# Kernel optimization log

Hardware: AMD Instinct MI355X
Metric: run time of the kernel (lower is better)

The kernel has to match this reference:

```python
import jax, jax.numpy as jnp
import numpy as np

COST_CLASS = 2.0
COST_MASK = 5.0
COST_DICE = 5.0
NUM_POINTS = 12544


def _point_sample(masks, coords):
    """Bilinear sample masks [N,H,W] at coords [P,2] in [0,1] (x,y order),
    matching F.grid_sample(align_corners=False, padding_mode='zeros')."""
    H, W = masks.shape[-2], masks.shape[-1]
    x = coords[:, 0] * W - 0.5  # [P]
    y = coords[:, 1] * H - 0.5
    x0 = jnp.floor(x)
    y0 = jnp.floor(y)
    wx = (x - x0).astype(masks.dtype)
    wy = (y - y0).astype(masks.dtype)
    x0i = x0.astype(jnp.int32)
    y0i = y0.astype(jnp.int32)

    def gather(xi, yi):
        valid = ((xi >= 0) & (xi < W) & (yi >= 0) & (yi < H)).astype(masks.dtype)
        xc = jnp.clip(xi, 0, W - 1)
        yc = jnp.clip(yi, 0, H - 1)
        return masks[:, yc, xc] * valid[None, :]  # [N,P]

    v00 = gather(x0i, y0i)
    v01 = gather(x0i + 1, y0i)
    v10 = gather(x0i, y0i + 1)
    v11 = gather(x0i + 1, y0i + 1)
    return (v00 * (1 - wx) * (1 - wy) + v01 * wx * (1 - wy)
            + v10 * (1 - wx) * wy + v11 * wx * wy)  # [N,P]


def setup_inputs() -> dict:
    key = jax.random.key(0)
    ks = jax.random.split(key, 6)
    B, Q, C, T, H, W = 8, 100, 41, 50, 256, 256
    return {
        "pred_logits": jax.random.normal(ks[0], (B, Q, C), jnp.float32),
        "pred_object_logits": jax.random.normal(ks[1], (B, Q, 2), jnp.float32),
        "pred_masks": jax.random.normal(ks[2], (B, Q, H, W), jnp.float32),
        "tgt_masks": jax.random.uniform(ks[3], (B, T, H, W), jnp.float32),
        "tgt_labels": jax.random.randint(ks[4], (B, T), 0, C),
        "point_coords": jax.random.uniform(ks[5], (B, NUM_POINTS, 2), jnp.float32),
    }


def reference(pred_logits, pred_object_logits, pred_masks, tgt_masks, tgt_labels, point_coords):
    B, Q, C = pred_logits.shape
    T = tgt_labels.shape[1]
    P = point_coords.shape[1]

    # --- class cost ---
    out_class_prob = jax.nn.sigmoid(pred_logits[..., :-1])          # [B,Q,C-1]
    out_object_prob = jax.nn.softmax(pred_object_logits, axis=-1)   # [B,Q,2]
    out_prob = jnp.concatenate(
        [jnp.sqrt(out_class_prob * out_object_prob[..., 0:1]),
         out_object_prob[..., 1:2]], axis=-1)                       # [B,Q,C]
    idx = jnp.broadcast_to(tgt_labels[:, None, :], (B, Q, T))
    cost_class = -jnp.take_along_axis(out_prob, idx, axis=2)        # [B,Q,T]

    # --- point-sample masks at shared random points ---
    om = jax.vmap(_point_sample)(pred_masks, point_coords)          # [B,Q,P]
    tm = jax.vmap(_point_sample)(tgt_masks, point_coords)           # [B,T,P]

    # --- batched sigmoid CE cost ---
    pos = jax.nn.softplus(-om)  # BCE vs target=1
    neg = jax.nn.softplus(om)   # BCE vs target=0
    cost_mask = (jnp.einsum('bqp,btp->bqt', pos, tm)
                 + jnp.einsum('bqp,btp->bqt', neg, 1.0 - tm)) / P

    # --- batched dice cost ---
    s = jax.nn.sigmoid(om)
    numerator = 2.0 * jnp.einsum('bqp,btp->bqt', s, tm)
    denominator = s.sum(-1)[:, :, None] + tm.sum(-1)[:, None, :]
    cost_dice = 1.0 - (numerator + 1.0) / (denominator + 1.0)

    Cmat = COST_MASK * cost_mask + COST_CLASS * cost_class + COST_DICE * cost_dice
    return Cmat  # [B,Q,T] batched assignment cost matrices
```

## Files before the change

### kernel.cpp

```cpp
#include <hip/hip_runtime.h>
#include <math.h>

#define BB 8
#define QQ 100
#define CC 41
#define TT 50
#define HH 256
#define WW 256
#define PP 12544
#define QP 112
#define TP 64
#define KS 8
#define KCH (PP / KS)

typedef _Float16 f16x8 __attribute__((ext_vector_type(8)));
typedef float f32x4 __attribute__((ext_vector_type(4)));

#if defined(__has_builtin)
#if __has_builtin(__builtin_amdgcn_cvt_pk_fp8_f32) && __has_builtin(__builtin_amdgcn_cvt_f32_fp8)
#define HAVE_FP8CVT 1
#endif
#endif

__device__ __forceinline__ unsigned int cvt1_e4m3_sw(float x) {
    unsigned int u = __float_as_uint(x);
    unsigned int s = (u >> 24) & 0x80u;
    float ax = fminf(fabsf(x), 448.f);
    if (ax < 0.015625f) {
        unsigned int m = (unsigned int)rintf(ax * 512.f);
        return s | m;
    }
    unsigned int v = __float_as_uint(ax);
    v += 0x7FFFFu + ((v >> 20) & 1u);
    int e = (int)(v >> 23) - 127;
    unsigned int m = (v >> 20) & 7u;
    if (e < -6) { m = (unsigned int)rintf(ax * 512.f); return s | m; }
    unsigned int ee = (unsigned int)(e + 7);
    if (ee >= 16u) { ee = 15u; m = 6u; }
    return s | (ee << 3) | m;
}

template <bool HI>
__device__ __forceinline__ unsigned int pack2_e4m3(float a, float b, unsigned int old) {
#ifdef HAVE_FP8CVT
    return (unsigned int)__builtin_amdgcn_cvt_pk_fp8_f32(a, b, (int)old, HI);
#else
    unsigned int p = (cvt1_e4m3_sw(a) | (cvt1_e4m3_sw(b) << 8)) << (HI ? 16 : 0);
    unsigned int mask = HI ? 0x0000FFFFu : 0xFFFF0000u;
    return (old & mask) | p;
#endif
}

__device__ __forceinline__ float e4m3_to_f32(unsigned int byte) {
#ifdef HAVE_FP8CVT
    return __builtin_amdgcn_cvt_f32_fp8((int)byte, 0);
#else
    unsigned int s = byte >> 7, e = (byte >> 3) & 15u, m = byte & 7u;
    float v = e ? __uint_as_float(((e + 120u) << 23) | (m << 20))
                : (float)m * 0.001953125f;
    return s ? -v : v;
#endif
}

__device__ __forceinline__ float samp(const unsigned char* __restrict__ mlds, float2 c) {
    float x = fmaf(c.x, 256.f, -0.5f);
    float y = fmaf(c.y, 256.f, -0.5f);
    float x0f = floorf(x), y0f = floorf(y);
    float wx = x - x0f, wy = y - y0f;
    int x0 = (int)x0f, y0 = (int)y0f;
    float fx0 = (x0 >= 0) ? 1.f : 0.f, fx1 = (x0 < 255) ? 1.f : 0.f;
    float fy0 = (y0 >= 0) ? 1.f : 0.f, fy1 = (y0 < 255) ? 1.f : 0.f;
    int x0c = max(x0, 0), x1c = min(x0 + 1, 255);
    int r0 = max(y0, 0) << 8, r1 = (min(y0 + 1, 255)) << 8;
    float v00 = e4m3_to_f32(mlds[r0 + x0c]);
    float v01 = e4m3_to_f32(mlds[r0 + x1c]);
    float v10 = e4m3_to_f32(mlds[r1 + x0c]);
    float v11 = e4m3_to_f32(mlds[r1 + x1c]);
    float wxa = (1.f - wx) * fx0, wxb = wx * fx1;
    float wya = (1.f - wy) * fy0, wyb = wy * fy1;
    return wya * fmaf(wxa, v00, wxb * v01) + wyb * fmaf(wxa, v10, wxb * v11);
}

__global__ __launch_bounds__(1024, 8) void sample_kernel(
    const float* __restrict__ tgt_masks, const float* __restrict__ pred_masks,
    const float* __restrict__ coords,
    _Float16* __restrict__ tm, _Float16* __restrict__ om, _Float16* __restrict__ sg,
    float* __restrict__ tmsum, float* __restrict__ nsum, float* __restrict__ ssum)
{
    __shared__ unsigned char mlds[HH * WW];
    __shared__ float red[16], red2[16];
    int id = blockIdx.x;
    int tid = threadIdx.x;
    bool is_t = id < BB * TT;
    int b;
    const float* m;
    _Float16* dst;
    _Float16* dsg = nullptr;
    if (is_t) {
        b = id / TT;
        m = tgt_masks + (size_t)id * (HH * WW);
        dst = tm + ((size_t)b * TP + (id % TT)) * PP;
    } else {
        int bq = id - BB * TT;
        b = bq / QQ;
        int q = bq % QQ;
        m = pred_masks + (size_t)bq * (HH * WW);
        dst = om + ((size_t)b * QP + q) * PP;
        dsg = sg + ((size_t)b * QP + q) * PP;
    }
    const float2* cd = (const float2*)coords + (size_t)b * PP;

    {
        const float4* s4 = (const float4*)m;
        unsigned int* dl = (unsigned int*)mlds;
        float4 v0 = s4[tid], v1 = s4[tid + 1024], v2 = s4[tid + 2048], v3 = s4[tid + 3072];
        float4 v4 = s4[tid + 4096], v5 = s4[tid + 5120], v6 = s4[tid + 6144], v7 = s4[tid + 7168];
        unsigned int pk;
        pk = pack2_e4m3<false>(v0.x, v0.y, 0u); dl[tid]        = pack2_e4m3<true>(v0.z, v0.w, pk);
        pk = pack2_e4m3<false>(v1.x, v1.y, 0u); dl[tid + 1024] = pack2_e4m3<true>(v1.z, v1.w, pk);
        pk = pack2_e4m3<false>(v2.x, v2.y, 0u); dl[tid + 2048] = pack2_e4m3<true>(v2.z, v2.w, pk);
        pk = pack2_e4m3<false>(v3.x, v3.y, 0u); dl[tid + 3072] = pack2_e4m3<true>(v3.z, v3.w, pk);
        pk = pack2_e4m3<false>(v4.x, v4.y, 0u); dl[tid + 4096] = pack2_e4m3<true>(v4.z, v4.w, pk);
        pk = pack2_e4m3<false>(v5.x, v5.y, 0u); dl[tid + 5120] = pack2_e4m3<true>(v5.z, v5.w, pk);
        pk = pack2_e4m3<false>(v6.x, v6.y, 0u); dl[tid + 6144] = pack2_e4m3<true>(v6.z, v6.w, pk);
        pk = pack2_e4m3<false>(v7.x, v7.y, 0u); dl[tid + 7168] = pack2_e4m3<true>(v7.z, v7.w, pk);
        float4 u0 = s4[tid + 8192], u1 = s4[tid + 9216], u2 = s4[tid + 10240], u3 = s4[tid + 11264];
        float4 u4 = s4[tid + 12288], u5 = s4[tid + 13312], u6 = s4[tid + 14336], u7 = s4[tid + 15360];
        pk = pack2_e4m3<false>(u0.x, u0.y, 0u); dl[tid + 8192]  = pack2_e4m3<true>(u0.z, u0.w, pk);
        pk = pack2_e4m3<false>(u1.x, u1.y, 0u); dl[tid + 9216]  = pack2_e4m3<true>(u1.z, u1.w, pk);
        pk = pack2_e4m3<false>(u2.x, u2.y, 0u); dl[tid + 10240] = pack2_e4m3<true>(u2.z, u2.w, pk);
        pk = pack2_e4m3<false>(u3.x, u3.y, 0u); dl[tid + 11264] = pack2_e4m3<true>(u3.z, u3.w, pk);
        pk = pack2_e4m3<false>(u4.x, u4.y, 0u); dl[tid + 12288] = pack2_e4m3<true>(u4.z, u4.w, pk);
        pk = pack2_e4m3<false>(u5.x, u5.y, 0u); dl[tid + 13312] = pack2_e4m3<true>(u5.z, u5.w, pk);
        pk = pack2_e4m3<false>(u6.x, u6.y, 0u); dl[tid + 14336] = pack2_e4m3<true>(u6.z, u6.w, pk);
        pk = pack2_e4m3<false>(u7.x, u7.y, 0u); dl[tid + 15360] = pack2_e4m3<true>(u7.z, u7.w, pk);
    }
    __syncthreads();

    float sA = 0.f, sB = 0.f;
    float nA = 0.f, nB = 0.f;
    float gA = 0.f, gB = 0.f;

    if (is_t) {
        #pragma unroll
        for (int g = 0; g < 3; ++g) {
            int p0 = g * 4096 + tid;
            float2 c0 = cd[p0], c1 = cd[p0 + 1024], c2 = cd[p0 + 2048], c3 = cd[p0 + 3072];
            float v0 = samp(mlds, c0), v1 = samp(mlds, c1);
            float v2 = samp(mlds, c2), v3 = samp(mlds, c3);
            dst[p0] = (_Float16)v0;
            dst[p0 + 1024] = (_Float16)v1;
            dst[p0 + 2048] = (_Float16)v2;
            dst[p0 + 3072] = (_Float16)v3;
            sA += v0 + v2; sB += v1 + v3;
        }
        if (tid < 256) {
            int p = 12288 + tid;
            float v = samp(mlds, cd[p]);
            dst[p] = (_Float16)v;
            sA += v;
        }
    } else {
        #pragma unroll
        for (int g = 0; g < 3; ++g) {
            int p0 = g * 4096 + tid;
            float2 c0 = cd[p0], c1 = cd[p0 + 1024], c2 = cd[p0 + 2048], c3 = cd[p0 + 3072];
            float v0 = samp(mlds, c0), v1 = samp(mlds, c1);
            float v2 = samp(mlds, c2), v3 = samp(mlds, c3);
            dst[p0] = (_Float16)v0;
            dst[p0 + 1024] = (_Float16)v1;
            dst[p0 + 2048] = (_Float16)v2;
            dst[p0 + 3072] = (_Float16)v3;
            float e0 = __expf(-fabsf(v0)), e1 = __expf(-fabsf(v1));
            float e2 = __expf(-fabsf(v2)), e3 = __expf(-fabsf(v3));
            float r0 = 1.f / (1.f + e0), r1 = 1.f / (1.f + e1);
            float r2 = 1.f / (1.f + e2), r3 = 1.f / (1.f + e3);
            float g0 = (v0 >= 0.f) ? r0 : e0 * r0, g1 = (v1 >= 0.f) ? r1 : e1 * r1;
            float g2 = (v2 >= 0.f) ? r2 : e2 * r2, g3 = (v3 >= 0.f) ? r3 : e3 * r3;
            dsg[p0] = (_Float16)g0;
            dsg[p0 + 1024] = (_Float16)g1;
            dsg[p0 + 2048] = (_Float16)g2;
            dsg[p0 + 3072] = (_Float16)g3;
            nA += fmaxf(v0, 0.f) + __logf(1.f + e0) + fmaxf(v2, 0.f) + __logf(1.f + e2);
            nB += fmaxf(v1, 0.f) + __logf(1.f + e1) + fmaxf(v3, 0.f) + __logf(1.f + e3);
            gA += g0 + g2; gB += g1 + g3;
        }
        if (tid < 256) {
            int p = 12288 + tid;
            float v = samp(mlds, cd[p]);
            dst[p] = (_Float16)v;
            float e = __expf(-fabsf(v));
            float r = 1.f / (1.f + e);
            float gg = (v >= 0.f) ? r : e * r;
            dsg[p] = (_Float16)gg;
            nA += fmaxf(v, 0.f) + __logf(1.f + e);
            gA += gg;
        }
    }

    float l1 = is_t ? (sA + sB) : (nA + nB);
    float l2 = gA + gB;
    #pragma unroll
    for (int off = 32; off; off >>= 1) {
        l1 += __shfl_down(l1, off, 64);
        l2 += __shfl_down(l2, off, 64);
    }
    if ((tid & 63) == 0) { red[tid >> 6] = l1; red2[tid >> 6] = l2; }
    __syncthreads();
    if (tid == 0) {
        float t1 = 0.f, t2 = 0.f;
        #pragma unroll
        for (int w = 0; w < 16; ++w) { t1 += red[w]; t2 += red2[w]; }
        if (is_t) tmsum[id] = t1;
        else { nsum[id - BB * TT] = t1; ssum[id - BB * TT] = t2; }
    }
}

__global__ __launch_bounds__(256) void dot_mfma_kernel(
    const _Float16* __restrict__ om, const _Float16* __restrict__ sg,
    const _Float16* __restrict__ tm,
    float* __restrict__ part_om, float* __restrict__ part_s)
{
    int qt = blockIdx.x, b = blockIdx.y, ks = blockIdx.z;
    int tid = threadIdx.x, lane = tid & 63, w = tid >> 6;
    int ra = lane & 15;
    int ko = (lane >> 4) * 8;
    const _Float16* pa = om + ((size_t)(b * QP + qt * 16 + ra)) * PP + ks * KCH + ko;
    const _Float16* ps = sg + ((size_t)(b * QP + qt * 16 + ra)) * PP + ks * KCH + ko;
    const _Float16* pb = tm + ((size_t)(b * TP + w * 16 + ra)) * PP + ks * KCH + ko;
    f32x4 accO = {0.f, 0.f, 0.f, 0.f};
    f32x4 accS = {0.f, 0.f, 0.f, 0.f};
    #pragma unroll 7
    for (int k = 0; k < KCH / 32; ++k) {
        f16x8 a = *(const f16x8*)(pa + (size_t)k * 32);
        f16x8 s = *(const f16x8*)(ps + (size_t)k * 32);
        f16x8 bb = *(const f16x8*)(pb + (size_t)k * 32);
        accO = __builtin_amdgcn_mfma_f32_16x16x32_f16(a, bb, accO, 0, 0, 0);
        accS = __builtin_amdgcn_mfma_f32_16x16x32_f16(s, bb, accS, 0, 0, 0);
    }
    int t = w * 16 + ra;
    int q = qt * 16 + (lane >> 4) * 4;
    size_t base = (((size_t)ks * BB + b) * QP + q) * TP + t;
    #pragma unroll
    for (int r = 0; r < 4; ++r) {
        part_om[base + (size_t)r * TP] = accO[r];
        part_s[base + (size_t)r * TP] = accS[r];
    }
}

__global__ __launch_bounds__(256) void epilogue_kernel(
    const float* __restrict__ part_om, const float* __restrict__ part_s,
    const float* __restrict__ tmsum, const float* __restrict__ nsum,
    const float* __restrict__ ssum, const float* __restrict__ pred_logits,
    const float* __restrict__ pred_obj, const int* __restrict__ labels,
    float* __restrict__ out)
{
    int i = blockIdx.x * 256 + threadIdx.x;
    if (i >= BB * QQ * TT) return;
    int t = i % TT;
    int bq = i / TT;
    int b = bq / QQ, q = bq % QQ;
    float dO = 0.f, dS = 0.f;
    #pragma unroll
    for (int ks = 0; ks < KS; ++ks) {
        size_t o = (((size_t)ks * BB + b) * QP + q) * TP + t;
        dO += part_om[o];
        dS += part_s[o];
    }
    float ns = nsum[bq], ss = ssum[bq];
    float ts = tmsum[b * TT + t];
    float cmask = (ns - dO) * (1.f / PP);
    float cdice = 1.f - (2.f * dS + 1.f) / (ss + ts + 1.f);
    int label = labels[b * TT + t];
    float a0 = pred_obj[bq * 2], a1 = pred_obj[bq * 2 + 1];
    float prob;
    if (label == CC - 1) {
        prob = 1.f / (1.f + __expf(a0 - a1));
    } else {
        float pc = 1.f / (1.f + __expf(-pred_logits[(size_t)bq * CC + label]));
        float po = 1.f / (1.f + __expf(a1 - a0));
        prob = sqrtf(pc * po);
    }
    out[i] = 5.f * cmask - 2.f * prob + 5.f * cdice;
}

extern "C" void kernel_launch(void* const* d_in, const int* in_sizes, int n_in,
                              void* d_out, int out_size, void* d_ws, size_t ws_size,
                              hipStream_t stream) {
    const float* pred_logits = (const float*)d_in[0];
    const float* pred_obj    = (const float*)d_in[1];
    const float* pred_masks  = (const float*)d_in[2];
    const float* tgt_masks   = (const float*)d_in[3];
    const int*   tgt_labels  = (const int*)d_in[4];
    const float* coords      = (const float*)d_in[5];
    float* out = (float*)d_out;

    char* ws = (char*)d_ws;
    const size_t SZ_OM = (size_t)BB * QP * PP * 2;
    const size_t SZ_TM = (size_t)BB * TP * PP * 2;
    const size_t SZ_PT = (size_t)KS * BB * QP * TP * 4;
    _Float16* om  = (_Float16*)ws;
    _Float16* sg  = (_Float16*)(ws + SZ_OM);
    _Float16* tmm = (_Float16*)(ws + 2 * SZ_OM);
    float* part_om = (float*)(ws + 2 * SZ_OM + SZ_TM);
    float* part_s  = (float*)(ws + 2 * SZ_OM + SZ_TM + SZ_PT);
    float* tmsum   = (float*)(ws + 2 * SZ_OM + SZ_TM + 2 * SZ_PT);
    float* nsum    = tmsum + BB * TT;
    float* ssum    = nsum + BB * QQ;

    hipLaunchKernelGGL(sample_kernel, dim3(BB * TT + BB * QQ), dim3(1024), 0, stream,
                       tgt_masks, pred_masks, coords, tmm, om, sg, tmsum, nsum, ssum);
    hipLaunchKernelGGL(dot_mfma_kernel, dim3(QP / 16, BB, KS), dim3(256), 0, stream,
                       om, sg, tmm, part_om, part_s);
    hipLaunchKernelGGL(epilogue_kernel, dim3((BB * QQ * TT + 255) / 256), dim3(256),
                       0, stream,
                       part_om, part_s, tmsum, nsum, ssum,
                       pred_logits, pred_obj, tgt_labels, out);
}
```

Before: 120.3 us.

## Make sample kernel persistent with double-buffered LDS prefetch of next mask

Each block of the sampling kernel now processes five masks in sequence using two 64KB LDS buffers. It loads the next mask from global memory into registers while sampling the current one, then packs it to fp8 into the other buffer. The aim is to overlap the global mask reads with gather/sampling compute. In exchange, LDS per block doubles, limiting residency to one block per CU, and the grid shrinks to 240 blocks, which may leave CUs idle.

Measured after the change: 124.4 us. 3.5% more time.

```diff
diff --git a/kernel.cpp b/kernel.cpp
--- a/kernel.cpp
+++ b/kernel.cpp
@@ -5,13 +5,15 @@
 #define QQ 100
 #define CC 41
 #define TT 50
-#define HH 256
-#define WW 256
 #define PP 12544
 #define QP 112
 #define TP 64
 #define KS 8
 #define KCH (PP / KS)
+#define NT (BB * TT)
+#define NMASK (NT + BB * QQ)
+#define MPB 5
+#define SGRID (NMASK / MPB)
 
 typedef _Float16 f16x8 __attribute__((ext_vector_type(8)));
 typedef float f32x4 __attribute__((ext_vector_type(4)));
@@ -62,7 +64,8 @@
 #endif
 }
 
-__device__ __forceinline__ float samp(const unsigned char* __restrict__ mlds, float2 c) {
+__device__ __forceinline__ void addr_w(float2 c, int& a00, int& a01, int& a10, int& a11,
+                                       float& xa, float& xb, float& ya, float& yb) {
     float x = fmaf(c.x, 256.f, -0.5f);
     float y = fmaf(c.y, 256.f, -0.5f);
     float x0f = floorf(x), y0f = floorf(y);
@@ -71,148 +74,152 @@
     float fx0 = (x0 >= 0) ? 1.f : 0.f, fx1 = (x0 < 255) ? 1.f : 0.f;
     float fy0 = (y0 >= 0) ? 1.f : 0.f, fy1 = (y0 < 255) ? 1.f : 0.f;
     int x0c = max(x0, 0), x1c = min(x0 + 1, 255);
-    int r0 = max(y0, 0) << 8, r1 = (min(y0 + 1, 255)) << 8;
-    float v00 = e4m3_to_f32(mlds[r0 + x0c]);
-    float v01 = e4m3_to_f32(mlds[r0 + x1c]);
-    float v10 = e4m3_to_f32(mlds[r1 + x0c]);
-    float v11 = e4m3_to_f32(mlds[r1 + x1c]);
-    float wxa = (1.f - wx) * fx0, wxb = wx * fx1;
-    float wya = (1.f - wy) * fy0, wyb = wy * fy1;
-    return wya * fmaf(wxa, v00, wxb * v01) + wyb * fmaf(wxa, v10, wxb * v11);
-}
-
-__global__ __launch_bounds__(1024, 8) void sample_kernel(
+    int r0 = max(y0, 0) << 8, r1 = min(y0 + 1, 255) << 8;
+    a00 = r0 + x0c; a01 = r0 + x1c; a10 = r1 + x0c; a11 = r1 + x1c;
+    xa = (1.f - wx) * fx0; xb = wx * fx1;
+    ya = (1.f - wy) * fy0; yb = wy * fy1;
+}
+
+__global__ __launch_bounds__(1024, 4) void sample_kernel(
     const float* __restrict__ tgt_masks, const float* __restrict__ pred_masks,
     const float* __restrict__ coords,
     _Float16* __restrict__ tm, _Float16* __restrict__ om, _Float16* __restrict__ sg,
     float* __restrict__ tmsum, float* __restrict__ nsum, float* __restrict__ ssum)
 {
-    __shared__ unsigned char mlds[HH * WW];
+    __shared__ unsigned int buf[2][16384];
     __shared__ float red[16], red2[16];
-    int id = blockIdx.x;
     int tid = threadIdx.x;
-    bool is_t = id < BB * TT;
-    int b;
-    const float* m;
-    _Float16* dst;
-    _Float16* dsg = nullptr;
-    if (is_t) {
-        b = id / TT;
-        m = tgt_masks + (size_t)id * (HH * WW);
-        dst = tm + ((size_t)b * TP + (id % TT)) * PP;
-    } else {
-        int bq = id - BB * TT;
-        b = bq / QQ;
-        int q = bq % QQ;
-        m = pred_masks + (size_t)bq * (HH * WW);
-        dst = om + ((size_t)b * QP + q) * PP;
-        dsg = sg + ((size_t)b * QP + q) * PP;
-    }
-    const float2* cd = (const float2*)coords + (size_t)b * PP;
+    int base = blockIdx.x * MPB;
 
     {
-        const float4* s4 = (const float4*)m;
-        unsigned int* dl = (unsigned int*)mlds;
-        float4 v0 = s4[tid], v1 = s4[tid + 1024], v2 = s4[tid + 2048], v3 = s4[tid + 3072];
-        float4 v4 = s4[tid + 4096], v5 = s4[tid + 5120], v6 = s4[tid + 6144], v7 = s4[tid + 7168];
-        unsigned int pk;
-        pk = pack2_e4m3<false>(v0.x, v0.y, 0u); dl[tid]        = pack2_e4m3<true>(v0.z, v0.w, pk);
-        pk = pack2_e4m3<false>(v1.x, v1.y, 0u); dl[tid + 1024] = pack2_e4m3<true>(v1.z, v1.w, pk);
-        pk = pack2_e4m3<false>(v2.x, v2.y, 0u); dl[tid + 2048] = pack2_e4m3<true>(v2.z, v2.w, pk);
-        pk = pack2_e4m3<false>(v3.x, v3.y, 0u); dl[tid + 3072] = pack2_e4m3<true>(v3.z, v3.w, pk);
-        pk = pack2_e4m3<false>(v4.x, v4.y, 0u); dl[tid + 4096] = pack2_e4m3<true>(v4.z, v4.w, pk);
-        pk = pack2_e4m3<false>(v5.x, v5.y, 0u); dl[tid + 5120] = pack2_e4m3<true>(v5.z, v5.w, pk);
-        pk = pack2_e4m3<false>(v6.x, v6.y, 0u); dl[tid + 6144] = pack2_e4m3<true>(v6.z, v6.w, pk);
-        pk = pack2_e4m3<false>(v7.x, v7.y, 0u); dl[tid + 7168] = pack2_e4m3<true>(v7.z, v7.w, pk);
-        float4 u0 = s4[tid + 8192], u1 = s4[tid + 9216], u2 = s4[tid + 10240], u3 = s4[tid + 11264];
-        float4 u4 = s4[tid + 12288], u5 = s4[tid + 13312], u6 = s4[tid + 14336], u7 = s4[tid + 15360];
-        pk = pack2_e4m3<false>(u0.x, u0.y, 0u); dl[tid + 8192]  = pack2_e4m3<true>(u0.z, u0.w, pk);
-        pk = pack2_e4m3<false>(u1.x, u1.y, 0u); dl[tid + 9216]  = pack2_e4m3<true>(u1.z, u1.w, pk);
-        pk = pack2_e4m3<false>(u2.x, u2.y, 0u); dl[tid + 10240] = pack2_e4m3<true>(u2.z, u2.w, pk);
-        pk = pack2_e4m3<false>(u3.x, u3.y, 0u); dl[tid + 11264] = pack2_e4m3<true>(u3.z, u3.w, pk);
-        pk = pack2_e4m3<false>(u4.x, u4.y, 0u); dl[tid + 12288] = pack2_e4m3<true>(u4.z, u4.w, pk);
-        pk = pack2_e4m3<false>(u5.x, u5.y, 0u); dl[tid + 13312] = pack2_e4m3<true>(u5.z, u5.w, pk);
-        pk = pack2_e4m3<false>(u6.x, u6.y, 0u); dl[tid + 14336] = pack2_e4m3<true>(u6.z, u6.w, pk);
-        pk = pack2_e4m3<false>(u7.x, u7.y, 0u); dl[tid + 15360] = pack2_e4m3<true>(u7.z, u7.w, pk);
+        const float* m0 = (base < NT) ? tgt_masks + (size_t)base * 65536
+                                      : pred_masks + (size_t)(base - NT) * 65536;
+        const float4* s4 = (const float4*)m0;
+        for (int half = 0; half < 2; ++half) {
+            float4 r[8];
+            #pragma unroll
+            for (int k = 0; k < 8; ++k) r[k] = s4[half * 8192 + k * 1024 + tid];
+            #pragma unroll
+            for (int k = 0; k < 8; ++k) {
+                unsigned int pk = pack2_e4m3<false>(r[k].x, r[k].y, 0u);
+                buf[0][half * 8192 + k * 1024 + tid] = pack2_e4m3<true>(r[k].z, r[k].w, pk);
+            }
+        }
     }
     __syncthreads();
 
-    float sA = 0.f, sB = 0.f;
-    float nA = 0.f, nB = 0.f;
-    float gA = 0.f, gB = 0.f;
-
-    if (is_t) {
+    for (int j = 0; j < MPB; ++j) {
+        int id = base + j;
+        bool is_t = id < NT;
+        int b;
+        _Float16* dst;
+        _Float16* dsg = nullptr;
+        if (is_t) {
+            b = id / TT;
+            dst = tm + ((size_t)b * TP + (id % TT)) * PP;
+        } else {
+            int bq = id - NT;
+            b = bq / QQ;
+            dst = om + ((size_t)b * QP + (bq % QQ)) * PP;
+            dsg = sg + ((size_t)b * QP + (bq % QQ)) * PP;
+        }
+        const float2* cd = (const float2*)coords + (size_t)b * PP;
+        const unsigned char* curb = (const unsigned char*)buf[j & 1];
+        unsigned int* nxt = buf[(j + 1) & 1];
+        bool has_next = (j + 1 < MPB);
+        const float4* ns4 = nullptr;
+        if (has_next) {
+            int nid = id + 1;
+            ns4 = (const float4*)((nid < NT) ? tgt_masks + (size_t)nid * 65536
+                                             : pred_masks + (size_t)(nid - NT) * 65536);
+        }
+
+        float l1 = 0.f, l2 = 0.f;
+        for (int half = 0; half < 2; ++half) {
+            float4 r[8];
+            if (has_next) {
+                #pragma unroll
+                for (int k = 0; k < 8; ++k) r[k] = ns4[half * 8192 + k * 1024 + tid];
+            }
+            #pragma unroll
+            for (int pr = 0; pr < 3; ++pr) {
+                int p1 = (half * 6 + pr * 2) * 1024 + tid;
+                int p2 = p1 + 1024;
+                float2 c1 = cd[p1], c2 = cd[p2];
+                int a00, a01, a10, a11, e00, e01, e10, e11;
+                float xa1, xb1, ya1, yb1, xa2, xb2, ya2, yb2;
+                addr_w(c1, a00, a01, a10, a11, xa1, xb1, ya1, yb1);
+                addr_w(c2, e00, e01, e10, e11, xa2, xb2, ya2, yb2);
+                unsigned int u00 = curb[a00], u01 = curb[a01];
+                unsigned int u10 = curb[a10], u11 = curb[a11];
+                unsigned int w00 = curb[e00], w01 = curb[e01];
+                unsigned int w10 = curb[e10], w11 = curb[e11];
+                float v1 = ya1 * fmaf(xa1, e4m3_to_f32(u00), xb1 * e4m3_to_f32(u01))
+                         + yb1 * fmaf(xa1, e4m3_to_f32(u10), xb1 * e4m3_to_f32(u11));
+                float v2 = ya2 * fmaf(xa2, e4m3_to_f32(w00), xb2 * e4m3_to_f32(w01))
+                         + yb2 * fmaf(xa2, e4m3_to_f32(w10), xb2 * e4m3_to_f32(w11));
+                dst[p1] = (_Float16)v1;
+                dst[p2] = (_Float16)v2;
+                if (is_t) {
+                    l1 += v1 + v2;
+                } else {
+                    float e1 = __expf(-fabsf(v1)), e2 = __expf(-fabsf(v2));
+                    float q1 = 1.f / (1.f + e1), q2 = 1.f / (1.f + e2);
+                    float g1 = (v1 >= 0.f) ? q1 : e1 * q1;
+                    float g2 = (v2 >= 0.f) ? q2 : e2 * q2;
+                    dsg[p1] = (_Float16)g1;
+                    dsg[p2] = (_Float16)g2;
+                    l1 += fmaxf(v1, 0.f) + __logf(1.f + e1)
+                        + fmaxf(v2, 0.f) + __logf(1.f + e2);
+                    l2 += g1 + g2;
+                }
+            }
+            if (half == 1 && tid < 256) {
+                int p = 12288 + tid;
+                float2 c = cd[p];
+                int a00, a01, a10, a11;
+                float xa, xb, ya, yb;
+                addr_w(c, a00, a01, a10, a11, xa, xb, ya, yb);
+                float v = ya * fmaf(xa, e4m3_to_f32((unsigned int)curb[a00]),
+                                    xb * e4m3_to_f32((unsigned int)curb[a01]))
+                        + yb * fmaf(xa, e4m3_to_f32((unsigned int)curb[a10]),
+                                    xb * e4m3_to_f32((unsigned int)curb[a11]));
+                dst[p] = (_Float16)v;
+                if (is_t) {
+                    l1 += v;
+                } else {
+                    float e = __expf(-fabsf(v));
+                    float q = 1.f / (1.f + e);
+                    float g = (v >= 0.f) ? q : e * q;
+                    dsg[p] = (_Float16)g;
+                    l1 += fmaxf(v, 0.f) + __logf(1.f + e);
+                    l2 += g;
+                }
+            }
+            if (has_next) {
+                #pragma unroll
+                for (int k = 0; k < 8; ++k) {
+                    unsigned int pk = pack2_e4m3<false>(r[k].x, r[k].y, 0u);
+                    nxt[half * 8192 + k * 1024 + tid] = pack2_e4m3<true>(r[k].z, r[k].w, pk);
+                }
+            }
+        }
+
         #pragma unroll
-        for (int g = 0; g < 3; ++g) {
-            int p0 = g * 4096 + tid;
-            float2 c0 = cd[p0], c1 = cd[p0 + 1024], c2 = cd[p0 + 2048], c3 = cd[p0 + 3072];
-            float v0 = samp(mlds, c0), v1 = samp(mlds, c1);
-            float v2 = samp(mlds, c2), v3 = samp(mlds, c3);
-            dst[p0] = (_Float16)v0;
-            dst[p0 + 1024] = (_Float16)v1;
-            dst[p0 + 2048] = (_Float16)v2;
-            dst[p0 + 3072] = (_Float16)v3;
-            sA += v0 + v2; sB += v1 + v3;
-        }
-        if (tid < 256) {
-            int p = 12288 + tid;
-            float v = samp(mlds, cd[p]);
-            dst[p] = (_Float16)v;
-            sA += v;
-        }
-    } else {
-        #pragma unroll
-        for (int g = 0; g < 3; ++g) {
-            int p0 = g * 4096 + tid;
-            float2 c0 = cd[p0], c1 = cd[p0 + 1024], c2 = cd[p0 + 2048], c3 = cd[p0 + 3072];
-            float v0 = samp(mlds, c0), v1 = samp(mlds, c1);
-            float v2 = samp(mlds, c2), v3 = samp(mlds, c3);
-            dst[p0] = (_Float16)v0;
-            dst[p0 + 1024] = (_Float16)v1;
-            dst[p0 + 2048] = (_Float16)v2;
-            dst[p0 + 3072] = (_Float16)v3;
-            float e0 = __expf(-fabsf(v0)), e1 = __expf(-fabsf(v1));
-            float e2 = __expf(-fabsf(v2)), e3 = __expf(-fabsf(v3));
-            float r0 = 1.f / (1.f + e0), r1 = 1.f / (1.f + e1);
-            float r2 = 1.f / (1.f + e2), r3 = 1.f / (1.f + e3);
-            float g0 = (v0 >= 0.f) ? r0 : e0 * r0, g1 = (v1 >= 0.f) ? r1 : e1 * r1;
-            float g2 = (v2 >= 0.f) ? r2 : e2 * r2, g3 = (v3 >= 0.f) ? r3 : e3 * r3;
-            dsg[p0] = (_Float16)g0;
-            dsg[p0 + 1024] = (_Float16)g1;
-            dsg[p0 + 2048] = (_Float16)g2;
-            dsg[p0 + 3072] = (_Float16)g3;
-            nA += fmaxf(v0, 0.f) + __logf(1.f + e0) + fmaxf(v2, 0.f) + __logf(1.f + e2);
-            nB += fmaxf(v1, 0.f) + __logf(1.f + e1) + fmaxf(v3, 0.f) + __logf(1.f + e3);
-            gA += g0 + g2; gB += g1 + g3;
-        }
-        if (tid < 256) {
-            int p = 12288 + tid;
-            float v = samp(mlds, cd[p]);
-            dst[p] = (_Float16)v;
-            float e = __expf(-fabsf(v));
-            float r = 1.f / (1.f + e);
-            float gg = (v >= 0.f) ? r : e * r;
-            dsg[p] = (_Float16)gg;
-            nA += fmaxf(v, 0.f) + __logf(1.f + e);
-            gA += gg;
-        }
-    }
-
-    float l1 = is_t ? (sA + sB) : (nA + nB);
-    float l2 = gA + gB;
-    #pragma unroll
-    for (int off = 32; off; off >>= 1) {
-        l1 += __shfl_down(l1, off, 64);
-        l2 += __shfl_down(l2, off, 64);
-    }
-    if ((tid & 63) == 0) { red[tid >> 6] = l1; red2[tid >> 6] = l2; }
-    __syncthreads();
-    if (tid == 0) {
-        float t1 = 0.f, t2 = 0.f;
-        #pragma unroll
-        for (int w = 0; w < 16; ++w) { t1 += red[w]; t2 += red2[w]; }
-        if (is_t) tmsum[id] = t1;
-        else { nsum[id - BB * TT] = t1; ssum[id - BB * TT] = t2; }
+        for (int off = 32; off; off >>= 1) {
+            l1 += __shfl_down(l1, off, 64);
+            l2 += __shfl_down(l2, off, 64);
+        }
+        if ((tid & 63) == 0) { red[tid >> 6] = l1; red2[tid >> 6] = l2; }
+        __syncthreads();
+        if (tid == 0) {
+            float t1 = 0.f, t2 = 0.f;
+            #pragma unroll
+            for (int w = 0; w < 16; ++w) { t1 += red[w]; t2 += red2[w]; }
+            if (is_t) tmsum[id] = t1;
+            else { nsum[id - NT] = t1; ssum[id - NT] = t2; }
+        }
+        __syncthreads();
     }
 }
 
@@ -240,11 +247,11 @@
     }
     int t = w * 16 + ra;
     int q = qt * 16 + (lane >> 4) * 4;
-    size_t base = (((size_t)ks * BB + b) * QP + q) * TP + t;
+    size_t bse = (((size_t)ks * BB + b) * QP + q) * TP + t;
     #pragma unroll
     for (int r = 0; r < 4; ++r) {
-        part_om[base + (size_t)r * TP] = accO[r];
-        part_s[base + (size_t)r * TP] = accS[r];
+        part_om[bse + (size_t)r * TP] = accO[r];
+        part_s[bse + (size_t)r * TP] = accS[r];
     }
 }
 
@@ -308,7 +315,7 @@
     float* nsum    = tmsum + BB * TT;
     float* ssum    = nsum + BB * QQ;
 
-    hipLaunchKernelGGL(sample_kernel, dim3(BB * TT + BB * QQ), dim3(1024), 0, stream,
+    hipLaunchKernelGGL(sample_kernel, dim3(SGRID), dim3(1024), 0, stream,
                        tgt_masks, pred_masks, coords, tmm, om, sg, tmsum, nsum, ssum);
     hipLaunchKernelGGL(dot_mfma_kernel, dim3(QP / 16, BB, KS), dim3(256), 0, stream,
                        om, sg, tmm, part_om, part_s);
```
